# Kernel tuning notes

Measured on AMD Instinct MI355X. Metric: run time of the kernel, lower is better.

## Reference

```python
import jax, jax.numpy as jnp
import numpy as np

N_AQI = 35
N_MEO = 18
H = N_AQI + 3 * N_MEO  # 89
T = 120
B = 32768


def setup_inputs() -> dict:
    key = jax.random.key(0)
    ks = jax.random.split(key, 9)
    s = 1.0 / np.sqrt(H)
    return {
        "out": jax.random.normal(ks[0], (B, T, H), dtype=jnp.float32),
        # GRUCell params (PyTorch layout: [3H, in], gate order r,z,n)
        "W_ih": jax.random.normal(ks[1], (3 * H, H), dtype=jnp.float32) * s,
        "W_hh": jax.random.normal(ks[2], (3 * H, H), dtype=jnp.float32) * s,
        "b_ih": jax.random.normal(ks[3], (3 * H,), dtype=jnp.float32) * s,
        "b_hh": jax.random.normal(ks[4], (3 * H,), dtype=jnp.float32) * s,
        # metric_fc: 89 -> 32
        "W_m": jax.random.normal(ks[5], (32, H), dtype=jnp.float32) * s,
        "b_m": jax.random.normal(ks[6], (32,), dtype=jnp.float32) * s,
        # output_fc: 32 -> 1
        "W_o": jax.random.normal(ks[7], (1, 32), dtype=jnp.float32) * (1.0 / np.sqrt(32)),
        "b_o": jax.random.normal(ks[8], (1,), dtype=jnp.float32) * (1.0 / np.sqrt(32)),
    }


def reference(out, W_ih, W_hh, b_ih, b_hh, W_m, b_m, W_o, b_o):
    h0 = jnp.zeros((out.shape[0], H), dtype=out.dtype)
    xs = jnp.transpose(out[:, :T, :], (1, 0, 2))  # (T, B, H)

    def step(h, x):
        gi = x @ W_ih.T + b_ih          # (B, 3H)
        gh = h @ W_hh.T + b_hh          # (B, 3H)
        i_r, i_z, i_n = jnp.split(gi, 3, axis=-1)
        h_r, h_z, h_n = jnp.split(gh, 3, axis=-1)
        r = jax.nn.sigmoid(i_r + h_r)
        z = jax.nn.sigmoid(i_z + h_z)
        n = jnp.tanh(i_n + r * h_n)
        h_new = (1.0 - z) * n + z * h   # PyTorch GRUCell update
        return h_new, None

    h, _ = jax.lax.scan(step, h0, xs)
    out_mmetric = jax.nn.sigmoid(h @ W_m.T + b_m)        # (B, 32)
    out_mscore = jax.nn.sigmoid(out_mmetric @ W_o.T + b_o)  # (B, 1)
    return out_mscore, out_mmetric
```

## Files before the change

kernel.cpp:

```cpp
#include <hip/hip_runtime.h>
#include <hip/hip_bf16.h>

#define Hn   89
#define Tn   120
#define BM   128
#define LDP  104
#define NTHR 768

using bf16   = __bf16;
using bf16x4 = __attribute__((ext_vector_type(4))) __bf16;
using bf16x8 = __attribute__((ext_vector_type(8))) __bf16;
typedef __attribute__((ext_vector_type(4))) float f32x4;

__device__ __forceinline__ f32x4 ld4(const float* p) {
  f32x4 v; __builtin_memcpy(&v, p, 16); return v;
}
__device__ __forceinline__ float fsig(float x) {
  return __builtin_amdgcn_rcpf(1.f + __builtin_amdgcn_exp2f(-1.44269504f * x));
}
__device__ __forceinline__ float ftanh(float x) {
  return 1.f - 2.f * __builtin_amdgcn_rcpf(1.f + __builtin_amdgcn_exp2f(2.88539008f * x));
}

__global__ __launch_bounds__(NTHR, 3)
void gru_fused(const float* __restrict__ X,
               const float* __restrict__ Wih,
               const float* __restrict__ Whh,
               const float* __restrict__ bih,
               const float* __restrict__ bhh,
               const float* __restrict__ Wm,
               const float* __restrict__ bm,
               const float* __restrict__ Wo,
               const float* __restrict__ bo,
               float* __restrict__ Y,
               int Bt)
{
  __shared__ __align__(16) bf16 Xl[2][BM][LDP];
  __shared__ __align__(16) bf16 Hl[2][BM][LDP];
  __shared__ float Ml[BM][32];

  const int tid  = threadIdx.x;
  const int lane = tid & 63;
  const int wv   = tid >> 6;
  const int jt   = wv >> 1;
  const int hf   = wv & 1;
  const int l15  = lane & 15;
  const int kg   = lane >> 4;
  const int j    = jt * 16 + l15;
  const bool jok = (j < Hn);
  const size_t brow0 = (size_t)blockIdx.x * BM;

  bf16x8 Bf[3][2][3];
#pragma unroll
  for (int g = 0; g < 3; ++g)
#pragma unroll
    for (int s = 0; s < 2; ++s) {
      const float* W = s ? Whh : Wih;
#pragma unroll
      for (int kt = 0; kt < 3; ++kt) {
        bf16x8 f;
        const int k0 = kt * 32 + kg * 8;
#pragma unroll
        for (int e = 0; e < 8; ++e) {
          const int k = k0 + e;
          float v = 0.f;
          if (jok) {
            if (k < Hn) v = W[(size_t)(g * Hn + j) * Hn + k];
            else if (k == Hn) {
              if (g < 2) v = s ? 0.f : (bih[g * Hn + j] + bhh[g * Hn + j]);
              else       v = s ? bhh[2 * Hn + j] : bih[2 * Hn + j];
            }
          }
          f[e] = (bf16)v;
        }
        Bf[g][s][kt] = f;
      }
    }

  int soff[4], loff[4];
  bool val[4], lst[4];
#pragma unroll
  for (int i = 0; i < 4; ++i) {
    const int p = tid + i * NTHR;
    const int r = p / 23, s = p - r * 23;
    val[i]  = (p < BM * 23);
    lst[i]  = (s == 22);
    soff[i] = r * (Tn * Hn) + s * 4;
    loff[i] = r * LDP + s * 4;
  }
  const float* Xb2 = X + brow0 * (size_t)(Tn * Hn);
  f32x4 pa[4];

  auto issue = [&](int tHv) {
#pragma unroll
    for (int i = 0; i < 4; ++i) {
      if (val[i]) {
        if (lst[i]) { f32x4 v = {Xb2[soff[i] + tHv], 1.0f, 0.f, 0.f}; pa[i] = v; }
        else          pa[i] = ld4(Xb2 + soff[i] + tHv);
      }
    }
  };

  if (tid < 2 * BM) {
    const int bb = tid >> 7, r = tid & (BM - 1);
    Hl[bb][r][89] = (bf16)1.0f;
#pragma unroll
    for (int c = 90; c < 96; ++c) Hl[bb][r][c] = (bf16)0.f;
#pragma unroll
    for (int c = 92; c < 96; ++c) Xl[bb][r][c] = (bf16)0.f;
  }

  float hold[4][4];
#pragma unroll
  for (int mt = 0; mt < 4; ++mt)
#pragma unroll
    for (int q = 0; q < 4; ++q) hold[mt][q] = 0.f;

  bf16*       hwb = &Hl[0][0][0] + (hf * 64 + kg * 4) * LDP + j;
  const bf16* xrb = &Xl[0][0][0] + (hf * 64 + l15) * LDP + kg * 8;
  const bf16* hrb = &Hl[0][0][0] + (hf * 64 + l15) * LDP + kg * 8;
  const int bufo = BM * LDP;

  issue(0);
  int tH = 0;
  for (int t = 0; t < Tn; ++t) {
    const int b = t & 1;
#pragma unroll
    for (int i = 0; i < 4; ++i) {
      if (val[i]) {
        bf16x4 w;
        w[0] = (bf16)pa[i][0]; w[1] = (bf16)pa[i][1];
        w[2] = (bf16)pa[i][2]; w[3] = (bf16)pa[i][3];
        *(bf16x4*)(&Xl[b][0][0] + loff[i]) = w;
      }
    }
    if (jok) {
      bf16* hw = hwb + b * bufo;
#pragma unroll
      for (int mt = 0; mt < 4; ++mt)
#pragma unroll
        for (int q = 0; q < 4; ++q)
          hw[(mt * 16 + q) * LDP] = (bf16)hold[mt][q];
    }
    __syncthreads();
    tH += Hn;
    if (t + 1 < Tn) issue(tH);

    const bf16* xr = xrb + b * bufo;
    const bf16* hr = hrb + b * bufo;
#pragma unroll
    for (int mt = 0; mt < 4; ++mt) {
      f32x4 ar = {0,0,0,0}, az = {0,0,0,0}, ain = {0,0,0,0}, ahn = {0,0,0,0};
#pragma unroll
      for (int kt = 0; kt < 3; ++kt) {
        const bf16x8 ax = *(const bf16x8*)(xr + mt * 16 * LDP + kt * 32);
        const bf16x8 ah = *(const bf16x8*)(hr + mt * 16 * LDP + kt * 32);
        ar  = __builtin_amdgcn_mfma_f32_16x16x32_bf16(ax, Bf[0][0][kt], ar, 0, 0, 0);
        ar  = __builtin_amdgcn_mfma_f32_16x16x32_bf16(ah, Bf[0][1][kt], ar, 0, 0, 0);
        az  = __builtin_amdgcn_mfma_f32_16x16x32_bf16(ax, Bf[1][0][kt], az, 0, 0, 0);
        az  = __builtin_amdgcn_mfma_f32_16x16x32_bf16(ah, Bf[1][1][kt], az, 0, 0, 0);
        ain = __builtin_amdgcn_mfma_f32_16x16x32_bf16(ax, Bf[2][0][kt], ain, 0, 0, 0);
        ahn = __builtin_amdgcn_mfma_f32_16x16x32_bf16(ah, Bf[2][1][kt], ahn, 0, 0, 0);
      }
#pragma unroll
      for (int q = 0; q < 4; ++q) {
        const float r_ = fsig(ar[q]);
        const float z_ = fsig(az[q]);
        const float n_ = ftanh(ain[q] + r_ * ahn[q]);
        hold[mt][q] = n_ + z_ * (hold[mt][q] - n_);
      }
    }
  }

  if (jok) {
#pragma unroll
    for (int mt = 0; mt < 4; ++mt)
#pragma unroll
      for (int q = 0; q < 4; ++q)
        hwb[(mt * 16 + q) * LDP] = (bf16)hold[mt][q];
  }
  __syncthreads();

  const bf16* Hf = &Hl[0][0][0];
  for (int p = tid; p < BM * 32; p += NTHR) {
    const int r = p >> 5, c = p & 31;
    float acc = bm[c];
    const bf16* hr2 = Hf + r * LDP;
    for (int k = 0; k < Hn; ++k) acc = fmaf((float)hr2[k], Wm[c * Hn + k], acc);
    const float mv = fsig(acc);
    Ml[r][c] = mv;
    Y[(size_t)Bt + (brow0 + r) * 32 + c] = mv;
  }
  __syncthreads();
  if (tid < BM) {
    float acc = bo[0];
#pragma unroll
    for (int c = 0; c < 32; ++c) acc = fmaf(Ml[tid][c], Wo[c], acc);
    Y[brow0 + tid] = fsig(acc);
  }
}

extern "C" void kernel_launch(void* const* d_in, const int* in_sizes, int n_in,
                              void* d_out, int out_size, void* d_ws, size_t ws_size,
                              hipStream_t stream) {
  const float* X   = (const float*)d_in[0];
  const float* Wih = (const float*)d_in[1];
  const float* Whh = (const float*)d_in[2];
  const float* bih = (const float*)d_in[3];
  const float* bhh = (const float*)d_in[4];
  const float* Wm  = (const float*)d_in[5];
  const float* bm  = (const float*)d_in[6];
  const float* Wo  = (const float*)d_in[7];
  const float* bo  = (const float*)d_in[8];

  const int B = in_sizes[0] / (Tn * Hn);
  dim3 grid(B / BM), block(NTHR);
  gru_fused<<<grid, block, 0, stream>>>(X, Wih, Whh, bih, bhh, Wm, bm, Wo, bo,
                                        (float*)d_out, B);
}
```

Measured before the change: 728.2 us.

## Restructure GRU step: swizzle H tile, write h in-loop, widen X loads

Hidden-state writes now happen inside the timestep's compute loop, going to the other LDS buffer. X prefetch uses two 8-wide loads per thread instead of four 4-wide ones, and is committed to LDS after compute, so each step needs only one barrier. The H tile gets an XOR swizzle on 8-element column groups to reduce LDS bank conflicts on the MFMA operand reads. s_setprio raises wave priority during the MFMA section, and the final metric FC is vectorised over the swizzled layout. The swizzle adds address arithmetic and makes the padding and bias-column indexing more intricate.

```diff
diff --git a/kernel.cpp b/kernel.cpp
--- a/kernel.cpp
+++ b/kernel.cpp
@@ -8,12 +8,17 @@
 #define NTHR 768
 
 using bf16   = __bf16;
-using bf16x4 = __attribute__((ext_vector_type(4))) __bf16;
 using bf16x8 = __attribute__((ext_vector_type(8))) __bf16;
 typedef __attribute__((ext_vector_type(4))) float f32x4;
 
 __device__ __forceinline__ f32x4 ld4(const float* p) {
   f32x4 v; __builtin_memcpy(&v, p, 16); return v;
+}
+__device__ __forceinline__ bf16x8 pack8(f32x4 a, f32x4 b) {
+  bf16x8 r;
+  r[0]=(bf16)a[0]; r[1]=(bf16)a[1]; r[2]=(bf16)a[2]; r[3]=(bf16)a[3];
+  r[4]=(bf16)b[0]; r[5]=(bf16)b[1]; r[6]=(bf16)b[2]; r[7]=(bf16)b[3];
+  return r;
 }
 __device__ __forceinline__ float fsig(float x) {
   return __builtin_amdgcn_rcpf(1.f + __builtin_amdgcn_exp2f(-1.44269504f * x));
@@ -48,6 +53,7 @@
   const int kg   = lane >> 4;
   const int j    = jt * 16 + l15;
   const bool jok = (j < Hn);
+  const int swz  = (l15 >> 2) & 3;
   const size_t brow0 = (size_t)blockIdx.x * BM;
 
   bf16x8 Bf[3][2][3];
@@ -77,37 +83,38 @@
       }
     }
 
-  int soff[4], loff[4];
-  bool val[4], lst[4];
-#pragma unroll
-  for (int i = 0; i < 4; ++i) {
-    const int p = tid + i * NTHR;
-    const int r = p / 23, s = p - r * 23;
-    val[i]  = (p < BM * 23);
-    lst[i]  = (s == 22);
-    soff[i] = r * (Tn * Hn) + s * 4;
-    loff[i] = r * LDP + s * 4;
+  int soff0, soff1, loff0, loff1;
+  bool lst0, lst1;
+  {
+    const int p0 = tid, p1 = tid + NTHR;
+    const int r0 = p0 / 12, s0 = p0 - r0 * 12;
+    const int r1 = p1 / 12, s1 = p1 - r1 * 12;
+    lst0 = (s0 == 11); lst1 = (s1 == 11);
+    soff0 = r0 * (Tn * Hn) + s0 * 8;  loff0 = r0 * LDP + s0 * 8;
+    soff1 = r1 * (Tn * Hn) + s1 * 8;  loff1 = r1 * LDP + s1 * 8;
   }
   const float* Xb2 = X + brow0 * (size_t)(Tn * Hn);
-  f32x4 pa[4];
-
-  auto issue = [&](int tHv) {
-#pragma unroll
-    for (int i = 0; i < 4; ++i) {
-      if (val[i]) {
-        if (lst[i]) { f32x4 v = {Xb2[soff[i] + tHv], 1.0f, 0.f, 0.f}; pa[i] = v; }
-        else          pa[i] = ld4(Xb2 + soff[i] + tHv);
-      }
-    }
+  f32x4 A0, B0, A1, B1;
+
+  auto issue = [&](int toff) {
+    const float* p0 = Xb2 + soff0 + toff;
+    const float* p1 = Xb2 + soff1 + toff;
+    if (lst0) { f32x4 a = {p0[0], 1.0f, 0.f, 0.f}; A0 = a; B0 = (f32x4){0.f,0.f,0.f,0.f}; }
+    else      { A0 = ld4(p0); B0 = ld4(p0 + 4); }
+    if (lst1) { f32x4 a = {p1[0], 1.0f, 0.f, 0.f}; A1 = a; B1 = (f32x4){0.f,0.f,0.f,0.f}; }
+    else      { A1 = ld4(p1); B1 = ld4(p1 + 4); }
   };
+  auto commit = [&](int plane) {
+    *(bf16x8*)(&Xl[plane][0][0] + loff0) = pack8(A0, B0);
+    *(bf16x8*)(&Xl[plane][0][0] + loff1) = pack8(A1, B1);
+  };
 
   if (tid < 2 * BM) {
-    const int bb = tid >> 7, r = tid & (BM - 1);
-    Hl[bb][r][89] = (bf16)1.0f;
-#pragma unroll
-    for (int c = 90; c < 96; ++c) Hl[bb][r][c] = (bf16)0.f;
-#pragma unroll
-    for (int c = 92; c < 96; ++c) Xl[bb][r][c] = (bf16)0.f;
+    const int pl = tid >> 7, r = tid & (BM - 1);
+    bf16* hp = &Hl[pl][r][(size_t)((11 ^ ((r >> 2) & 3)) << 3)];
+    hp[1] = (bf16)1.0f;
+#pragma unroll
+    for (int e = 2; e < 8; ++e) hp[e] = (bf16)0.f;
   }
 
   float hold[4][4];
@@ -116,38 +123,33 @@
 #pragma unroll
     for (int q = 0; q < 4; ++q) hold[mt][q] = 0.f;
 
-  bf16*       hwb = &Hl[0][0][0] + (hf * 64 + kg * 4) * LDP + j;
+  const int hswzcol = (((j >> 3) ^ kg) << 3) | (j & 7);
+  bf16*       hwb = &Hl[0][0][0] + (hf * 64 + kg * 4) * LDP + hswzcol;
   const bf16* xrb = &Xl[0][0][0] + (hf * 64 + l15) * LDP + kg * 8;
-  const bf16* hrb = &Hl[0][0][0] + (hf * 64 + l15) * LDP + kg * 8;
+  const bf16* hrb = &Hl[0][0][0] + (hf * 64 + l15) * LDP + ((kg ^ swz) << 3);
   const int bufo = BM * LDP;
 
   issue(0);
-  int tH = 0;
+  if (jok) {
+#pragma unroll
+    for (int mt = 0; mt < 4; ++mt)
+#pragma unroll
+      for (int q = 0; q < 4; ++q)
+        hwb[(mt * 16 + q) * LDP] = (bf16)0.f;
+  }
+  commit(0);
+
+  int toff = Hn;
   for (int t = 0; t < Tn; ++t) {
     const int b = t & 1;
-#pragma unroll
-    for (int i = 0; i < 4; ++i) {
-      if (val[i]) {
-        bf16x4 w;
-        w[0] = (bf16)pa[i][0]; w[1] = (bf16)pa[i][1];
-        w[2] = (bf16)pa[i][2]; w[3] = (bf16)pa[i][3];
-        *(bf16x4*)(&Xl[b][0][0] + loff[i]) = w;
-      }
-    }
-    if (jok) {
-      bf16* hw = hwb + b * bufo;
-#pragma unroll
-      for (int mt = 0; mt < 4; ++mt)
-#pragma unroll
-        for (int q = 0; q < 4; ++q)
-          hw[(mt * 16 + q) * LDP] = (bf16)hold[mt][q];
-    }
     __syncthreads();
-    tH += Hn;
-    if (t + 1 < Tn) issue(tH);
-
+    const bool pf = (t + 1 < Tn);
+    if (pf) issue(toff);
+
+    __builtin_amdgcn_s_setprio(1);
     const bf16* xr = xrb + b * bufo;
     const bf16* hr = hrb + b * bufo;
+    bf16*       hw = hwb + (b ^ 1) * bufo;
 #pragma unroll
     for (int mt = 0; mt < 4; ++mt) {
       f32x4 ar = {0,0,0,0}, az = {0,0,0,0}, ain = {0,0,0,0}, ahn = {0,0,0,0};
@@ -169,24 +171,34 @@
         const float n_ = ftanh(ain[q] + r_ * ahn[q]);
         hold[mt][q] = n_ + z_ * (hold[mt][q] - n_);
       }
+      if (jok) {
+#pragma unroll
+        for (int q = 0; q < 4; ++q)
+          hw[(mt * 16 + q) * LDP] = (bf16)hold[mt][q];
+      }
     }
-  }
-
-  if (jok) {
-#pragma unroll
-    for (int mt = 0; mt < 4; ++mt)
-#pragma unroll
-      for (int q = 0; q < 4; ++q)
-        hwb[(mt * 16 + q) * LDP] = (bf16)hold[mt][q];
+    __builtin_amdgcn_s_setprio(0);
+    if (pf) { commit(b ^ 1); toff += Hn; }
   }
   __syncthreads();
 
-  const bf16* Hf = &Hl[0][0][0];
   for (int p = tid; p < BM * 32; p += NTHR) {
     const int r = p >> 5, c = p & 31;
+    const int rs = (r >> 2) & 3;
+    const bf16* hr2 = &Hl[0][r][0];
+    const float* wrow = Wm + c * Hn;
     float acc = bm[c];
-    const bf16* hr2 = Hf + r * LDP;
-    for (int k = 0; k < Hn; ++k) acc = fmaf((float)hr2[k], Wm[c * Hn + k], acc);
+#pragma unroll 4
+    for (int cb = 0; cb < 11; ++cb) {
+      const bf16x8 hv = *(const bf16x8*)(hr2 + ((cb ^ rs) << 3));
+      const f32x4 wa = ld4(wrow + cb * 8);
+      const f32x4 wb = ld4(wrow + cb * 8 + 4);
+      acc = fmaf((float)hv[0], wa[0], acc); acc = fmaf((float)hv[1], wa[1], acc);
+      acc = fmaf((float)hv[2], wa[2], acc); acc = fmaf((float)hv[3], wa[3], acc);
+      acc = fmaf((float)hv[4], wb[0], acc); acc = fmaf((float)hv[5], wb[1], acc);
+      acc = fmaf((float)hv[6], wb[2], acc); acc = fmaf((float)hv[7], wb[3], acc);
+    }
+    acc = fmaf((float)hr2[(11 ^ rs) << 3], wrow[88], acc);
     const float mv = fsig(acc);
     Ml[r][c] = mv;
     Y[(size_t)Bt + (brow0 + r) * 32 + c] = mv;
```

After: 624.6 us. 14.2% less time.
